# Kernel optimization log

Measured on AMD Instinct MI355X. Metric: run time of the kernel, lower is better.

The kernel has to match this reference:

```python
import jax, jax.numpy as jnp
import numpy as np

MARGIN = 0.2
EPS = 1e-6  # torch.pairwise_distance adds eps to the difference before the norm


def setup_inputs() -> dict:
    key = jax.random.key(0)
    k1, k2, k3 = jax.random.split(key, 3)
    B, D = 8192, 128
    emb1 = jax.random.normal(k1, (B, D), dtype=jnp.float32)
    emb2 = jax.random.normal(k2, (B, D), dtype=jnp.float32)
    target = jax.random.randint(k3, (B,), 0, 2, dtype=jnp.int64)
    return {"emb1": emb1, "emb2": emb2, "target": target}


def reference(emb1, emb2, target):
    B, D = emb1.shape
    # torch.pairwise_distance(a, b) = ||a - b + EPS||_2; expand the square:
    # |a-b+eps|^2 = |a|^2 + |b|^2 - 2 a.b + 2*eps*(sum(a)-sum(b)) + D*eps^2
    sq = (
        jnp.sum(emb1 * emb1, axis=-1)[:, None]
        + jnp.sum(emb2 * emb2, axis=-1)[None, :]
        - 2.0 * (emb1 @ emb2.T)
        + 2.0 * EPS * (jnp.sum(emb1, axis=-1)[:, None] - jnp.sum(emb2, axis=-1)[None, :])
        + D * EPS * EPS
    )
    dist = jnp.sqrt(jnp.maximum(sq, 0.0))  # [B, B]: dist[i, j] = ||emb1[i] - emb2[j] + eps||

    pos = target == 1
    neg = target == 0
    # hardest positive: max over columns j with target[j]==1; hardest negative: min over target[j]==0
    pos_max = jnp.max(jnp.where(pos[None, :], dist, -jnp.inf), axis=1)  # [B]
    neg_min = jnp.min(jnp.where(neg[None, :], dist, jnp.inf), axis=1)   # [B]
    per_anchor = jnp.maximum(pos_max - neg_min + MARGIN, 0.0)
    anchor_w = pos.astype(dist.dtype)
    # mean over anchors (rows i with target[i]==1)
    return jnp.sum(per_anchor * anchor_w) / jnp.sum(anchor_w)
```

## Files before the change

### kernel.cpp

```cpp
#include <hip/hip_runtime.h>
#include <hip/hip_bf16.h>
#include <math.h>


#define DDIM   128
#define SPLITS 8
#define MARGIN 0.2f
#define EPS    1e-6f
#define SENT   1e30f

#define CHUNK_PITCH  1056
#define PANEL_CHUNKS 16
#define PANEL_BYTES  (PANEL_CHUNKS * CHUNK_PITCH)

typedef unsigned short ushort_t;
typedef __attribute__((ext_vector_type(8))) short short8;
typedef __attribute__((ext_vector_type(4))) float f32x4;
typedef __attribute__((ext_vector_type(4))) unsigned short ushort4_t;

__device__ __forceinline__ ushort_t f2bf(float f) {
    unsigned int u = __float_as_uint(f);
    u = (u + 0x7FFFu + ((u >> 16) & 1u)) >> 16;
    return (ushort_t)u;
}

__device__ __forceinline__ void g2lds16(const ushort_t* g, void* lds) {
    __builtin_amdgcn_global_load_lds(
        (const __attribute__((address_space(1))) unsigned int*)g,
        (__attribute__((address_space(3))) unsigned int*)lds,
        16, 0, 0);
}

__global__ void prep_kernel(const float* __restrict__ e1, const float* __restrict__ e2,
                            const int* __restrict__ target,
                            ushort_t* __restrict__ e1b, ushort_t* __restrict__ e2b,
                            float* __restrict__ rowterm,
                            float* __restrict__ cpos, float* __restrict__ cneg,
                            float* __restrict__ redsum, int* __restrict__ ticket, int B) {
    if (blockIdx.x == 0) {
        if (threadIdx.x == 0) { redsum[0] = 0.f; redsum[1] = 0.f; }
        else if (threadIdx.x == 1) *ticket = 0;
    }
    int gr  = blockIdx.x * 32 + (threadIdx.x >> 3);
    int seg = threadIdx.x & 7;
    bool first = gr < B;
    int r = first ? gr : gr - B;
    const float* src = (first ? e1 : e2) + (size_t)r * DDIM;
    ushort_t*    dst = (first ? e1b : e2b) + (size_t)r * DDIM;
    const float sc = first ? -2.f : 1.f;
    float s = 0.f, n = 0.f;
    #pragma unroll
    for (int it = 0; it < 4; ++it) {
        int e0 = (seg + it * 8) * 4;
        float4 v = *(const float4*)(src + e0);
        ushort4_t o;
        o.x = f2bf(sc * v.x); o.y = f2bf(sc * v.y);
        o.z = f2bf(sc * v.z); o.w = f2bf(sc * v.w);
        *(ushort4_t*)(dst + e0) = o;
        s += v.x + v.y + v.z + v.w;
        n += v.x * v.x + v.y * v.y + v.z * v.z + v.w * v.w;
    }
    #pragma unroll
    for (int m = 1; m <= 4; m <<= 1) {
        s += __shfl_xor(s, m, 64);
        n += __shfl_xor(n, m, 64);
    }
    if (seg == 0) {
        if (first) {
            rowterm[r] = n + 2.f * EPS * s + (float)DDIM * EPS * EPS;
        } else {
            float ct = n - 2.f * EPS * s;
            int tg = target[r];
            cpos[r] = (tg == 1) ? ct : -SENT;
            cneg[r] = (tg == 0) ? ct :  SENT;
        }
    }
}

__device__ __forceinline__ void stage_panel(const ushort_t* __restrict__ rowBase,
                                            unsigned char* __restrict__ lds,
                                            int w, int l, int sl) {
    const ushort_t* g = rowBase + (size_t)(w * 16 + (l >> 4)) * DDIM + sl * 8;
    unsigned char* lp = lds + (w * 4) * CHUNK_PITCH;
    #pragma unroll
    for (int it = 0; it < 4; ++it)
        g2lds16(g + it * 4 * DDIM, lp + it * CHUNK_PITCH);
}

__global__ __launch_bounds__(256, 3)
void tile_kernel(const ushort_t* __restrict__ e1b, const ushort_t* __restrict__ e2b,
                 const float* __restrict__ cpos, const float* __restrict__ cneg,
                 float* __restrict__ pmp, float* __restrict__ nmp, int B) {
    __shared__ __align__(16) unsigned char Bs[2][PANEL_BYTES];

    const int tid = threadIdx.x;
    const int w   = tid >> 6;
    const int l   = tid & 63;
    const int lq  = l >> 4;
    const int lm  = l & 15;
    const int row0 = blockIdx.x * 128;
    const int col0 = blockIdx.y * 1024;
    const int nPanels = 16;

    const int wr = (w >> 1) * 64;
    const int wc = (w & 1) * 32;

    const int sl = (l & 12) | ((l ^ (l >> 4)) & 3);

    stage_panel(e2b + (size_t)col0 * DDIM, Bs[0], w, l, sl);

    const ushort_t* aG = e1b + (size_t)(row0 + wr + lm) * DDIM + lq * 8;
    short8 afr[4][4];
    #pragma unroll
    for (int i = 0; i < 4; ++i)
        #pragma unroll
        for (int k4 = 0; k4 < 4; ++k4)
            afr[i][k4] = *(const short8*)(aG + i * 16 * DDIM + k4 * 32);

    const unsigned char* bLane = &Bs[0][0]
        + ((wc >> 2) + (lm >> 2)) * CHUNK_PITCH
        + (lm & 3) * 256 + ((lq ^ (lm & 3)) * 16);

    float pm[4][4], nm[4][4];
    #pragma unroll
    for (int i = 0; i < 4; ++i)
        #pragma unroll
        for (int r = 0; r < 4; ++r) { pm[i][r] = -SENT; nm[i][r] = SENT; }

    __syncthreads();

    for (int p = 0; p < nPanels; ++p) {
        if (p + 1 < nPanels)
            stage_panel(e2b + (size_t)(col0 + (p + 1) * 64) * DDIM,
                        Bs[(p + 1) & 1], w, l, sl);

        const unsigned char* bl = bLane + (p & 1) * PANEL_BYTES;

        f32x4 accA[4], accB[4];
        #pragma unroll
        for (int i = 0; i < 4; ++i) {
            accA[i] = (f32x4){0.f, 0.f, 0.f, 0.f};
            accB[i] = (f32x4){0.f, 0.f, 0.f, 0.f};
        }

        #pragma unroll
        for (int k4 = 0; k4 < 4; ++k4) {
            const short8 b0 = *(const short8*)(bl + k4 * 64);
            const short8 b1 = *(const short8*)(bl + 4 * CHUNK_PITCH + k4 * 64);
            #pragma unroll
            for (int i = 0; i < 4; ++i)
                accA[i] = __builtin_amdgcn_mfma_f32_16x16x32_bf16(
                              afr[i][k4], b0, accA[i], 0, 0, 0);
            #pragma unroll
            for (int i = 0; i < 4; ++i)
                accB[i] = __builtin_amdgcn_mfma_f32_16x16x32_bf16(
                              afr[i][k4], b1, accB[i], 0, 0, 0);
        }

        {
            const int colb = col0 + p * 64 + wc + lm;
            const float cp0 = cpos[colb],      cn0 = cneg[colb];
            const float cp1 = cpos[colb + 16], cn1 = cneg[colb + 16];
            #pragma unroll
            for (int i = 0; i < 4; ++i)
                #pragma unroll
                for (int r = 0; r < 4; ++r) {
                    const float d0 = accA[i][r];
                    const float d1 = accB[i][r];
                    pm[i][r] = fmaxf(fmaxf(pm[i][r], d0 + cp0), d1 + cp1);
                    nm[i][r] = fminf(fminf(nm[i][r], d0 + cn0), d1 + cn1);
                }
        }

        __syncthreads();
    }

    #pragma unroll
    for (int m = 1; m < 16; m <<= 1) {
        #pragma unroll
        for (int i = 0; i < 4; ++i)
            #pragma unroll
            for (int r = 0; r < 4; ++r) {
                pm[i][r] = fmaxf(pm[i][r], __shfl_xor(pm[i][r], m, 64));
                nm[i][r] = fminf(nm[i][r], __shfl_xor(nm[i][r], m, 64));
            }
    }

    float* smP = (float*)Bs;
    float* smN = smP + 128;
    if ((w & 1) == 1 && lm == 0) {
        #pragma unroll
        for (int i = 0; i < 4; ++i)
            #pragma unroll
            for (int r = 0; r < 4; ++r) {
                int lr = wr + i * 16 + lq * 4 + r;
                smP[lr] = pm[i][r];
                smN[lr] = nm[i][r];
            }
    }
    __syncthreads();
    if ((w & 1) == 0 && lm == 0) {
        #pragma unroll
        for (int i = 0; i < 4; ++i)
            #pragma unroll
            for (int r = 0; r < 4; ++r) {
                int lr = wr + i * 16 + lq * 4 + r;
                smP[lr] = fmaxf(pm[i][r], smP[lr]);
                smN[lr] = fminf(nm[i][r], smN[lr]);
            }
    }
    __syncthreads();
    if (tid < 128) {
        pmp[(size_t)blockIdx.y * B + row0 + tid] = smP[tid];
        nmp[(size_t)blockIdx.y * B + row0 + tid] = smN[tid];
    }
}

__global__ void reduce_kernel(const float* __restrict__ pmp, const float* __restrict__ nmp,
                              const float* __restrict__ rowterm, const int* __restrict__ target,
                              float* __restrict__ redsum, int* __restrict__ ticket,
                              float* __restrict__ out, int B) {
    int row = blockIdx.x * blockDim.x + threadIdx.x;
    float s = 0.f, c = 0.f;
    {
        float pmv = -SENT, nmv = SENT;
        #pragma unroll
        for (int sp = 0; sp < SPLITS; ++sp) {
            pmv = fmaxf(pmv, pmp[(size_t)sp * B + row]);
            nmv = fminf(nmv, nmp[(size_t)sp * B + row]);
        }
        float rt = rowterm[row];
        float dp = sqrtf(fmaxf(rt + pmv, 0.f));
        float dn = sqrtf(fmaxf(rt + nmv, 0.f));
        if (target[row] == 1) {
            s = fmaxf(dp - dn + MARGIN, 0.f);
            c = 1.f;
        }
    }
    #pragma unroll
    for (int off = 32; off > 0; off >>= 1) {
        s += __shfl_down(s, off, 64);
        c += __shfl_down(c, off, 64);
    }
    __shared__ float ls[4], lc[4];
    int wv = threadIdx.x >> 6, ln = threadIdx.x & 63;
    if (ln == 0) { ls[wv] = s; lc[wv] = c; }
    __syncthreads();
    if (threadIdx.x == 0) {
        float ss = ls[0] + ls[1] + ls[2] + ls[3];
        float cc = lc[0] + lc[1] + lc[2] + lc[3];
        atomicAdd(&redsum[0], ss);
        atomicAdd(&redsum[1], cc);
        __threadfence();
        int done = atomicAdd(ticket, 1);
        if (done == (int)gridDim.x - 1) {
            __threadfence();
            float fs = __hip_atomic_load(&redsum[0], __ATOMIC_RELAXED, __HIP_MEMORY_SCOPE_AGENT);
            float fc = __hip_atomic_load(&redsum[1], __ATOMIC_RELAXED, __HIP_MEMORY_SCOPE_AGENT);
            out[0] = fs / fc;
        }
    }
}

extern "C" void kernel_launch(void* const* d_in, const int* in_sizes, int n_in,
                              void* d_out, int out_size, void* d_ws, size_t ws_size,
                              hipStream_t stream) {
    const float* e1     = (const float*)d_in[0];
    const float* e2     = (const float*)d_in[1];
    const int*   target = (const int*)d_in[2];
    float* out = (float*)d_out;
    const int B = in_sizes[2];

    char* p = (char*)d_ws;
    ushort_t* e1b  = (ushort_t*)p;   p += (size_t)B * DDIM * 2;
    ushort_t* e2b  = (ushort_t*)p;   p += (size_t)B * DDIM * 2;
    float* rowterm = (float*)p;      p += (size_t)B * 4;
    float* cpos    = (float*)p;      p += (size_t)B * 4;
    float* cneg    = (float*)p;      p += (size_t)B * 4;
    float* pmp     = (float*)p;      p += (size_t)SPLITS * B * 4;
    float* nmp     = (float*)p;      p += (size_t)SPLITS * B * 4;
    float* redsum  = (float*)p;      p += 2 * 4;
    int*   ticket  = (int*)p;

    {
        int blocks = (2 * B) / 32;
        prep_kernel<<<blocks, 256, 0, stream>>>(e1, e2, target, e1b, e2b,
                                                rowterm, cpos, cneg,
                                                redsum, ticket, B);
    }
    {
        dim3 grid(B / 128, SPLITS);
        tile_kernel<<<grid, 256, 0, stream>>>(e1b, e2b, cpos, cneg, pmp, nmp, B);
    }
    reduce_kernel<<<32, 256, 0, stream>>>(pmp, nmp, rowterm, target,
                                          redsum, ticket, out, B);
}
```

Baseline: 91.11 us.

## Stage column terms in LDS and use explicit waitcnt barriers for panel pipeline

The per-column cpos/cneg terms for the block's 1024 columns are now loaded once into LDS through direct global-to-LDS loads, replacing per-panel global reads. The end-of-panel __syncthreads is replaced by raw s_barrier calls and a partial vmcnt wait, so the next panel's prefetch stays in flight while the current panel is consumed. This is meant to cut global load latency and over-conservative waits from the inner loop. LDS use grows by 8 KB, which may limit occupancy, and the hand-placed waitcnt and barrier ordering is fragile.

```diff
diff --git a/kernel.cpp b/kernel.cpp
--- a/kernel.cpp
+++ b/kernel.cpp
@@ -12,6 +12,7 @@
 #define CHUNK_PITCH  1056
 #define PANEL_CHUNKS 16
 #define PANEL_BYTES  (PANEL_CHUNKS * CHUNK_PITCH)
+#define CPCN_BYTES   (2048 * 4)
 
 typedef unsigned short ushort_t;
 typedef __attribute__((ext_vector_type(8))) short short8;
@@ -24,7 +25,7 @@
     return (ushort_t)u;
 }
 
-__device__ __forceinline__ void g2lds16(const ushort_t* g, void* lds) {
+__device__ __forceinline__ void g2lds16(const void* g, void* lds) {
     __builtin_amdgcn_global_load_lds(
         (const __attribute__((address_space(1))) unsigned int*)g,
         (__attribute__((address_space(3))) unsigned int*)lds,
@@ -91,7 +92,11 @@
 void tile_kernel(const ushort_t* __restrict__ e1b, const ushort_t* __restrict__ e2b,
                  const float* __restrict__ cpos, const float* __restrict__ cneg,
                  float* __restrict__ pmp, float* __restrict__ nmp, int B) {
-    __shared__ __align__(16) unsigned char Bs[2][PANEL_BYTES];
+    __shared__ __align__(16) unsigned char smRaw[2 * PANEL_BYTES + CPCN_BYTES];
+    unsigned char* Bs0  = smRaw;
+    unsigned char* Bs1  = smRaw + PANEL_BYTES;
+    float*         smCp = (float*)(smRaw + 2 * PANEL_BYTES);
+    float*         smCn = smCp + 1024;
 
     const int tid = threadIdx.x;
     const int w   = tid >> 6;
@@ -107,7 +112,9 @@
 
     const int sl = (l & 12) | ((l ^ (l >> 4)) & 3);
 
-    stage_panel(e2b + (size_t)col0 * DDIM, Bs[0], w, l, sl);
+    stage_panel(e2b + (size_t)col0 * DDIM, Bs0, w, l, sl);
+    g2lds16(cpos + col0 + w * 256 + l * 4, smCp + w * 256);
+    g2lds16(cneg + col0 + w * 256 + l * 4, smCn + w * 256);
 
     const ushort_t* aG = e1b + (size_t)(row0 + wr + lm) * DDIM + lq * 8;
     short8 afr[4][4];
@@ -117,7 +124,7 @@
         for (int k4 = 0; k4 < 4; ++k4)
             afr[i][k4] = *(const short8*)(aG + i * 16 * DDIM + k4 * 32);
 
-    const unsigned char* bLane = &Bs[0][0]
+    const unsigned char* bLane = Bs0
         + ((wc >> 2) + (lm >> 2)) * CHUNK_PITCH
         + (lm & 3) * 256 + ((lq ^ (lm & 3)) * 16);
 
@@ -130,9 +137,16 @@
     __syncthreads();
 
     for (int p = 0; p < nPanels; ++p) {
-        if (p + 1 < nPanels)
+        if (p) __builtin_amdgcn_s_barrier();
+
+        if (p + 1 < nPanels) {
             stage_panel(e2b + (size_t)(col0 + (p + 1) * 64) * DDIM,
-                        Bs[(p + 1) & 1], w, l, sl);
+                        (p & 1) ? Bs0 : Bs1, w, l, sl);
+            asm volatile("s_waitcnt vmcnt(4)" ::: "memory");
+        } else {
+            asm volatile("s_waitcnt vmcnt(0)" ::: "memory");
+        }
+        __builtin_amdgcn_s_barrier();
 
         const unsigned char* bl = bLane + (p & 1) * PANEL_BYTES;
 
@@ -158,9 +172,9 @@
         }
 
         {
-            const int colb = col0 + p * 64 + wc + lm;
-            const float cp0 = cpos[colb],      cn0 = cneg[colb];
-            const float cp1 = cpos[colb + 16], cn1 = cneg[colb + 16];
+            const int lcb = p * 64 + wc + lm;
+            const float cp0 = smCp[lcb],      cn0 = smCn[lcb];
+            const float cp1 = smCp[lcb + 16], cn1 = smCn[lcb + 16];
             #pragma unroll
             for (int i = 0; i < 4; ++i)
                 #pragma unroll
@@ -171,8 +185,6 @@
                     nm[i][r] = fminf(fminf(nm[i][r], d0 + cn0), d1 + cn1);
                 }
         }
-
-        __syncthreads();
     }
 
     #pragma unroll
@@ -186,7 +198,7 @@
             }
     }
 
-    float* smP = (float*)Bs;
+    float* smP = (float*)smRaw;
     float* smN = smP + 128;
     if ((w & 1) == 1 && lm == 0) {
         #pragma unroll
```

Result: no change. 89.68 us (median of 2 runs) (-1.6%).
